# Kernel optimization log

Hardware: AMD Instinct MI355X
Metric: run time of the kernel (lower is better)

The kernel has to match this reference:

```python
import jax, jax.numpy as jnp
import numpy as np

H = 64  # hidden size

def setup_inputs() -> dict:
    key = jax.random.key(0)
    ks = jax.random.split(key, 10)
    B, T = 8192, 256
    s = 1.0 / np.sqrt(H)  # torch LSTM/Linear init scale
    x = jax.random.normal(ks[0], (B, T, 1), dtype=jnp.float32)
    W_ih = jax.random.uniform(ks[1], (4 * H, 1), minval=-s, maxval=s, dtype=jnp.float32)
    W_hh = jax.random.uniform(ks[2], (4 * H, H), minval=-s, maxval=s, dtype=jnp.float32)
    b_ih = jax.random.uniform(ks[3], (4 * H,), minval=-s, maxval=s, dtype=jnp.float32)
    b_hh = jax.random.uniform(ks[4], (4 * H,), minval=-s, maxval=s, dtype=jnp.float32)
    fc1_w = jax.random.uniform(ks[5], (32, H), minval=-s, maxval=s, dtype=jnp.float32)
    fc1_b = jax.random.uniform(ks[6], (32,), minval=-s, maxval=s, dtype=jnp.float32)
    s2 = 1.0 / np.sqrt(32)
    fc2_w = jax.random.uniform(ks[7], (2, 32), minval=-s2, maxval=s2, dtype=jnp.float32)
    fc2_b = jax.random.uniform(ks[8], (2,), minval=-s2, maxval=s2, dtype=jnp.float32)
    return {"x": x, "W_ih": W_ih, "W_hh": W_hh, "b_ih": b_ih, "b_hh": b_hh,
            "fc1_w": fc1_w, "fc1_b": fc1_b, "fc2_w": fc2_w, "fc2_b": fc2_b}

def _lstm_last(x, W_ih, W_hh, b_ih, b_hh):
    # x: [B, T, 1]; returns final hidden state h_T: [B, H]
    B = x.shape[0]
    b = b_ih + b_hh
    x_t = jnp.swapaxes(x, 0, 1)  # [T, B, 1]
    # input contribution precomputed for all steps: [T, B, 4H]
    xg = jnp.einsum('tbi,gi->tbg', x_t, W_ih) + b
    def step(carry, xg_t):
        h, c = carry
        gates = xg_t + h @ W_hh.T  # [B, 4H]
        i, f, g, o = jnp.split(gates, 4, axis=-1)  # torch gate order i,f,g,o
        i = jax.nn.sigmoid(i); f = jax.nn.sigmoid(f)
        g = jnp.tanh(g); o = jax.nn.sigmoid(o)
        c = f * c + i * g
        h = o * jnp.tanh(c)
        return (h, c), None
    h0 = jnp.zeros((B, H), dtype=x.dtype)
    c0 = jnp.zeros((B, H), dtype=x.dtype)
    (h, _), _ = jax.lax.scan(step, (h0, c0), xg)
    return h

def reference(x, W_ih, W_hh, b_ih, b_hh, fc1_w, fc1_b, fc2_w, fc2_b):
    h = _lstm_last(x, W_ih, W_hh, b_ih, b_hh)          # lstm_out[:, -1, :] == h_n
    z = jax.nn.relu(h @ fc1_w.T + fc1_b)               # fc1 + relu
    return z @ fc2_w.T + fc2_b                          # fc2 -> [B, 2]
```

## Files before the change

kernel.cpp:

```cpp
#include <hip/hip_runtime.h>


typedef __attribute__((ext_vector_type(8))) _Float16 f16x8;
typedef __attribute__((ext_vector_type(4))) float f32x4;

#define TT 256
#define BT 16
#define XPAD 260

#if __has_builtin(__builtin_amdgcn_exp2f)
#define EXP2F __builtin_amdgcn_exp2f
#else
#define EXP2F exp2f
#endif
#if __has_builtin(__builtin_amdgcn_rcpf)
#define RCPF __builtin_amdgcn_rcpf
#else
#define RCPF(x) (1.0f / (x))
#endif
#if __has_builtin(__builtin_amdgcn_fmed3f)
#define MED3F __builtin_amdgcn_fmed3f
#else
#define MED3F(a, lo, hi) fminf(fmaxf((a), (lo)), (hi))
#endif

#define NLOG2E  -1.4426950408889634f
#define N2LOG2E -2.8853900817779268f

__device__ __forceinline__ ushort f2h_bits(float f) {
    union { _Float16 h; ushort u; } v;
    v.h = (_Float16)f;
    return v.u;
}
__device__ __forceinline__ float h2f(ushort u) {
    union { ushort u; _Float16 h; } v;
    v.u = u;
    return (float)v.h;
}

__global__ __launch_bounds__(1024, 8) void lstm_h16(
    const float* __restrict__ x,
    const float* __restrict__ W_ih,
    const float* __restrict__ W_hh,
    const float* __restrict__ b_ih,
    const float* __restrict__ b_hh,
    const float* __restrict__ fc1_w,
    const float* __restrict__ fc1_b,
    const float* __restrict__ fc2_w,
    const float* __restrict__ fc2_b,
    float* __restrict__ out)
{
    __shared__ float  x_lds[BT][XPAD];
    __shared__ ushort h_pl[2][BT * 64];

    const int tid  = threadIdx.x;
    const int lane = tid & 63;
    const int w    = tid >> 6;
    const int l15  = lane & 15;
    const int l4   = lane >> 4;
    const int s7   = l15 & 7;
    const long long bBase = (long long)blockIdx.x * BT;

    {
        const float4* xg = (const float4*)(x + bBase * TT);
        const int b = tid >> 6, c4 = tid & 63;
        *(float4*)&x_lds[b][c4 * 4] = xg[tid];
    }
    h_pl[0][tid] = 0;

    const int gate = l15 & 3;
    const int um   = w * 4 + (l15 >> 2);
    const float sgA = (gate == 2) ? N2LOG2E : NLOG2E;
    f16x8 Wf[2];
#pragma unroll
    for (int kt = 0; kt < 2; ++kt) {
        const float* src = W_hh + (gate * 64 + um) * 64 + kt * 32 + l4 * 8;
#pragma unroll
        for (int j = 0; j < 8; ++j)
            Wf[kt][j] = (_Float16)(src[j] * sgA);
    }

    const int u = 4 * w + l4;
    float wih[4], bias[4];
#pragma unroll
    for (int g = 0; g < 4; ++g) {
        const float sg = (g == 2) ? N2LOG2E : NLOG2E;
        const int idx = g * 64 + u;
        wih[g]  = W_ih[idx] * sg;
        bias[g] = (b_ih[idx] + b_hh[idx]) * sg;
    }

    const int ro = l15 * 64;
    const int b0 = l4 ^ s7;
    const int o0 = ro + b0 * 8;
    const int o1 = ro + (b0 ^ 4) * 8;
    const int wo = ro + (((w >> 1) ^ s7) << 3) + ((w & 1) << 2) + l4;

    float cst = 0.0f;
    __syncthreads();

    auto step = [&](int p, int t) {
        const f16x8 bh0 = *(const f16x8*)&h_pl[p][o0];
        const f16x8 bh1 = *(const f16x8*)&h_pl[p][o1];
        const float xr = x_lds[l15][t];

        f32x4 acc;
#pragma unroll
        for (int g = 0; g < 4; ++g) acc[g] = xr * wih[g] + bias[g];

        acc = __builtin_amdgcn_mfma_f32_16x16x32_f16(Wf[0], bh0, acc, 0, 0, 0);
        acc = __builtin_amdgcn_mfma_f32_16x16x32_f16(Wf[1], bh1, acc, 0, 0, 0);

        const float A  = EXP2F(acc[0]);
        const float F  = EXP2F(acc[1]);
        const float Bv = EXP2F(acc[2]);
        const float C  = EXP2F(acc[3]);
        const float pA = 1.0f + A, pF = 1.0f + F, pB = 1.0f + Bv, pC = 1.0f + C;
        const float P   = pA * pB;
        const float den = P * pF;
        const float num = cst * P + (1.0f - Bv) * pF;
        const float cc  = num * RCPF(den);
        cst = cc;
        const float targ = MED3F(N2LOG2E * cc, -60.0f, 60.0f);
        const float D  = EXP2F(targ);
        const float hn = (1.0f - D) * RCPF(pC * (1.0f + D));

        h_pl[p ^ 1][wo] = f2h_bits(hn);
        __syncthreads();
    };

#pragma unroll 1
    for (int t = 0; t < TT; t += 2) {
        step(0, t);
        step(1, t + 1);
    }

    if (tid < BT * 32) {
        const int b = tid >> 5, u2 = tid & 31;
        float a = fc1_b[u2];
        for (int k = 0; k < 64; ++k) {
            const int off = b * 64 + ((((k >> 3) ^ (b & 7))) << 3) + (k & 7);
            a += fc1_w[u2 * 64 + k] * h2f(h_pl[0][off]);
        }
        x_lds[b][u2] = a > 0.0f ? a : 0.0f;
    }
    __syncthreads();
    if (tid < BT * 2) {
        const int b = tid >> 1, o = tid & 1;
        float a = fc2_b[o];
#pragma unroll
        for (int u2 = 0; u2 < 32; ++u2)
            a += x_lds[b][u2] * fc2_w[o * 32 + u2];
        out[(bBase + b) * 2 + o] = a;
    }
}

extern "C" void kernel_launch(void* const* d_in, const int* in_sizes, int n_in,
                              void* d_out, int out_size, void* d_ws, size_t ws_size,
                              hipStream_t stream) {
    const float* x     = (const float*)d_in[0];
    const float* W_ih  = (const float*)d_in[1];
    const float* W_hh  = (const float*)d_in[2];
    const float* b_ih  = (const float*)d_in[3];
    const float* b_hh  = (const float*)d_in[4];
    const float* fc1_w = (const float*)d_in[5];
    const float* fc1_b = (const float*)d_in[6];
    const float* fc2_w = (const float*)d_in[7];
    const float* fc2_b = (const float*)d_in[8];
    float* out = (float*)d_out;

    lstm_h16<<<dim3(8192 / BT), dim3(1024), 0, stream>>>(
        x, W_ih, W_hh, b_ih, b_hh, fc1_w, fc1_b, fc2_w, fc2_b, out);
}
```

Measured before the change: 160.5 us.

## Switch LSTM recurrence to 32x32x16 MFMA with 32-sequence blocks

Each block now handles 32 batch rows with 512 threads (8 waves) and uses the 32x32x16 f16 MFMA. Each wave computes 8 hidden units by 4 gates for all 32 rows, so one lane now processes four cell states per step. This halves the number of blocks and per-step barriers relative to the work done, and amortises the LDS h reads over more rows. In exchange each thread carries more registers and does a longer serial gate computation per step, and each block syncs 8 waves instead of 16 per timestep.

```diff
diff --git a/kernel.cpp b/kernel.cpp
--- a/kernel.cpp
+++ b/kernel.cpp
@@ -2,10 +2,10 @@
 
 
 typedef __attribute__((ext_vector_type(8))) _Float16 f16x8;
-typedef __attribute__((ext_vector_type(4))) float f32x4;
+typedef __attribute__((ext_vector_type(16))) float f32x16;
 
 #define TT 256
-#define BT 16
+#define BT 32
 #define XPAD 260
 
 #if __has_builtin(__builtin_amdgcn_exp2f)
@@ -38,7 +38,7 @@
     return (float)v.h;
 }
 
-__global__ __launch_bounds__(1024, 8) void lstm_h16(
+__global__ __launch_bounds__(512, 2) void lstm_32(
     const float* __restrict__ x,
     const float* __restrict__ W_ih,
     const float* __restrict__ W_hh,
@@ -56,93 +56,110 @@
     const int tid  = threadIdx.x;
     const int lane = tid & 63;
     const int w    = tid >> 6;
-    const int l15  = lane & 15;
-    const int l4   = lane >> 4;
-    const int s7   = l15 & 7;
+    const int b31  = lane & 31;
+    const int hi   = lane >> 5;
+    const int s7   = b31 & 7;
     const long long bBase = (long long)blockIdx.x * BT;
 
     {
         const float4* xg = (const float4*)(x + bBase * TT);
-        const int b = tid >> 6, c4 = tid & 63;
-        *(float4*)&x_lds[b][c4 * 4] = xg[tid];
+        for (int i = tid; i < BT * TT / 4; i += 512) {
+            int b = i >> 6, c4 = i & 63;
+            *(float4*)&x_lds[b][c4 * 4] = xg[i];
+        }
     }
-    h_pl[0][tid] = 0;
+    ((unsigned long long*)h_pl[0])[tid] = 0ull;
 
-    const int gate = l15 & 3;
-    const int um   = w * 4 + (l15 >> 2);
-    const float sgA = (gate == 2) ? N2LOG2E : NLOG2E;
-    f16x8 Wf[2];
+    const int gateA = b31 & 3;
+    const int unitA = 8 * w + (b31 >> 2);
+    const float sgA = (gateA == 2) ? N2LOG2E : NLOG2E;
+    f16x8 Af[4];
 #pragma unroll
-    for (int kt = 0; kt < 2; ++kt) {
-        const float* src = W_hh + (gate * 64 + um) * 64 + kt * 32 + l4 * 8;
+    for (int kt = 0; kt < 4; ++kt) {
+        const float* src = W_hh + (gateA * 64 + unitA) * 64 + kt * 16 + hi * 8;
 #pragma unroll
         for (int j = 0; j < 8; ++j)
-            Wf[kt][j] = (_Float16)(src[j] * sgA);
+            Af[kt][j] = (_Float16)(src[j] * sgA);
     }
 
-    const int u = 4 * w + l4;
-    float wih[4], bias[4];
+    float wih[16], bias[16];
 #pragma unroll
-    for (int g = 0; g < 4; ++g) {
+    for (int r = 0; r < 16; ++r) {
+        const int g = r & 3, q = r >> 2;
+        const int u = 8 * w + 2 * q + hi;
         const float sg = (g == 2) ? N2LOG2E : NLOG2E;
         const int idx = g * 64 + u;
-        wih[g]  = W_ih[idx] * sg;
-        bias[g] = (b_ih[idx] + b_hh[idx]) * sg;
+        wih[r]  = W_ih[idx] * sg;
+        bias[r] = (b_ih[idx] + b_hh[idx]) * sg;
     }
 
-    const int ro = l15 * 64;
-    const int b0 = l4 ^ s7;
-    const int o0 = ro + b0 * 8;
-    const int o1 = ro + (b0 ^ 4) * 8;
-    const int wo = ro + (((w >> 1) ^ s7) << 3) + ((w & 1) << 2) + l4;
+    const int ro = b31 * 64;
+    int rdOff[4], wrOff[4];
+#pragma unroll
+    for (int kt = 0; kt < 4; ++kt)
+        rdOff[kt] = ro + (((2 * kt + hi) ^ s7) << 3);
+#pragma unroll
+    for (int q = 0; q < 4; ++q)
+        wrOff[q] = ro + ((w ^ s7) << 3) + 2 * q + hi;
 
-    float cst = 0.0f;
+    float cst[4] = {0.f, 0.f, 0.f, 0.f};
     __syncthreads();
 
-    auto step = [&](int p, int t) {
-        const f16x8 bh0 = *(const f16x8*)&h_pl[p][o0];
-        const f16x8 bh1 = *(const f16x8*)&h_pl[p][o1];
-        const float xr = x_lds[l15][t];
+    auto stepf = [&](int p, int t) {
+        const f16x8 B0 = *(const f16x8*)&h_pl[p][rdOff[0]];
+        const f16x8 B1 = *(const f16x8*)&h_pl[p][rdOff[1]];
+        const f16x8 B2 = *(const f16x8*)&h_pl[p][rdOff[2]];
+        const f16x8 B3 = *(const f16x8*)&h_pl[p][rdOff[3]];
+        const float xr = x_lds[b31][t];
 
-        f32x4 acc;
+        f32x16 acc;
 #pragma unroll
-        for (int g = 0; g < 4; ++g) acc[g] = xr * wih[g] + bias[g];
+        for (int r = 0; r < 16; ++r) acc[r] = xr * wih[r] + bias[r];
 
-        acc = __builtin_amdgcn_mfma_f32_16x16x32_f16(Wf[0], bh0, acc, 0, 0, 0);
-        acc = __builtin_amdgcn_mfma_f32_16x16x32_f16(Wf[1], bh1, acc, 0, 0, 0);
+        acc = __builtin_amdgcn_mfma_f32_32x32x16_f16(Af[0], B0, acc, 0, 0, 0);
+        acc = __builtin_amdgcn_mfma_f32_32x32x16_f16(Af[1], B1, acc, 0, 0, 0);
+        acc = __builtin_amdgcn_mfma_f32_32x32x16_f16(Af[2], B2, acc, 0, 0, 0);
+        acc = __builtin_amdgcn_mfma_f32_32x32x16_f16(Af[3], B3, acc, 0, 0, 0);
 
-        const float A  = EXP2F(acc[0]);
-        const float F  = EXP2F(acc[1]);
-        const float Bv = EXP2F(acc[2]);
-        const float C  = EXP2F(acc[3]);
-        const float pA = 1.0f + A, pF = 1.0f + F, pB = 1.0f + Bv, pC = 1.0f + C;
-        const float P   = pA * pB;
-        const float den = P * pF;
-        const float num = cst * P + (1.0f - Bv) * pF;
-        const float cc  = num * RCPF(den);
-        cst = cc;
-        const float targ = MED3F(N2LOG2E * cc, -60.0f, 60.0f);
-        const float D  = EXP2F(targ);
-        const float hn = (1.0f - D) * RCPF(pC * (1.0f + D));
-
-        h_pl[p ^ 1][wo] = f2h_bits(hn);
+#pragma unroll
+        for (int q = 0; q < 4; ++q) {
+            const float A_ = EXP2F(acc[4 * q + 0]);
+            const float F_ = EXP2F(acc[4 * q + 1]);
+            const float Bv = EXP2F(acc[4 * q + 2]);
+            const float C_ = EXP2F(acc[4 * q + 3]);
+            const float pA = 1.0f + A_, pF = 1.0f + F_, pB = 1.0f + Bv, pC = 1.0f + C_;
+            const float P   = pA * pB;
+            const float den = P * pF;
+            const float num = cst[q] * P + (1.0f - Bv) * pF;
+            const float cc  = num * RCPF(den);
+            cst[q] = cc;
+            const float targ = MED3F(N2LOG2E * cc, -60.0f, 60.0f);
+            const float D  = EXP2F(targ);
+            const float hn = (1.0f - D) * RCPF(pC * (1.0f + D));
+            h_pl[p ^ 1][wrOff[q]] = f2h_bits(hn);
+        }
         __syncthreads();
     };
 
 #pragma unroll 1
     for (int t = 0; t < TT; t += 2) {
-        step(0, t);
-        step(1, t + 1);
+        stepf(0, t);
+        stepf(1, t + 1);
     }
 
-    if (tid < BT * 32) {
-        const int b = tid >> 5, u2 = tid & 31;
-        float a = fc1_b[u2];
-        for (int k = 0; k < 64; ++k) {
-            const int off = b * 64 + ((((k >> 3) ^ (b & 7))) << 3) + (k & 7);
-            a += fc1_w[u2 * 64 + k] * h2f(h_pl[0][off]);
+    {
+        const int b = tid >> 4;
+        const int u2a = (tid & 15) * 2;
+#pragma unroll
+        for (int q2 = 0; q2 < 2; ++q2) {
+            const int u2 = u2a + q2;
+            float a = fc1_b[u2];
+            for (int k = 0; k < 64; ++k) {
+                const int off = b * 64 + ((((k >> 3) ^ (b & 7))) << 3) + (k & 7);
+                a += fc1_w[u2 * 64 + k] * h2f(h_pl[0][off]);
+            }
+            x_lds[b][u2] = a > 0.0f ? a : 0.0f;
         }
-        x_lds[b][u2] = a > 0.0f ? a : 0.0f;
     }
     __syncthreads();
     if (tid < BT * 2) {
@@ -169,6 +186,6 @@
     const float* fc2_b = (const float*)d_in[8];
     float* out = (float*)d_out;
 
-    lstm_h16<<<dim3(8192 / BT), dim3(1024), 0, stream>>>(
+    lstm_32<<<dim3(8192 / BT), dim3(512), 0, stream>>>(
         x, W_ih, W_hh, b_ih, b_hh, fc1_w, fc1_b, fc2_w, fc2_b, out);
 }
```

Result: slower. 178.8 us (+11.4%).

## Halve batch tile to 8 rows and use 8-wave blocks with two MFMAs per k-slice

Applied to the files above, without the earlier changes.

Changes the block to 512 threads handling 8 batch rows, so each wave computes 8 hidden units by issuing two MFMA tiles per k-slice. Only half of the 16 MFMA columns now carry useful batch rows, and each lane selects the accumulator it owns. The aim is a shorter per-step barrier over fewer waves and twice as many blocks, which may raise CU occupancy across the 256 serial steps. In exchange, half of the MFMA work is wasted and W_hh fragments double per thread, raising register pressure.

```diff
diff --git a/kernel.cpp b/kernel.cpp
--- a/kernel.cpp
+++ b/kernel.cpp
@@ -5,7 +5,7 @@
 typedef __attribute__((ext_vector_type(4))) float f32x4;
 
 #define TT 256
-#define BT 16
+#define BT 8
 #define XPAD 260
 
 #if __has_builtin(__builtin_amdgcn_exp2f)
@@ -38,7 +38,7 @@
     return (float)v.h;
 }
 
-__global__ __launch_bounds__(1024, 8) void lstm_h16(
+__global__ __launch_bounds__(512, 8) void lstm_g4(
     const float* __restrict__ x,
     const float* __restrict__ W_ih,
     const float* __restrict__ W_hh,
@@ -58,7 +58,8 @@
     const int w    = tid >> 6;
     const int l15  = lane & 15;
     const int l4   = lane >> 4;
-    const int s7   = l15 & 7;
+    const int r    = l15 & 7;
+    const bool own0 = (l15 < 8);
     const long long bBase = (long long)blockIdx.x * BT;
 
     {
@@ -68,54 +69,66 @@
     }
     h_pl[0][tid] = 0;
 
-    const int gate = l15 & 3;
-    const int um   = w * 4 + (l15 >> 2);
-    const float sgA = (gate == 2) ? N2LOG2E : NLOG2E;
-    f16x8 Wf[2];
+    const int gateA = l15 & 3;
+    const float sgA = (gateA == 2) ? N2LOG2E : NLOG2E;
+    f16x8 Af[2][2];
 #pragma unroll
-    for (int kt = 0; kt < 2; ++kt) {
-        const float* src = W_hh + (gate * 64 + um) * 64 + kt * 32 + l4 * 8;
+    for (int tt = 0; tt < 2; ++tt) {
+        const int unit = 8 * w + tt * 4 + (l15 >> 2);
 #pragma unroll
-        for (int j = 0; j < 8; ++j)
-            Wf[kt][j] = (_Float16)(src[j] * sgA);
+        for (int kt = 0; kt < 2; ++kt) {
+            const float* src = W_hh + (gateA * 64 + unit) * 64 + kt * 32 + l4 * 8;
+#pragma unroll
+            for (int j = 0; j < 8; ++j)
+                Af[tt][kt][j] = (_Float16)(src[j] * sgA);
+        }
     }
 
-    const int u = 4 * w + l4;
+    const int unit_o = 8 * w + (own0 ? 0 : 4) + l4;
     float wih[4], bias[4];
 #pragma unroll
     for (int g = 0; g < 4; ++g) {
         const float sg = (g == 2) ? N2LOG2E : NLOG2E;
-        const int idx = g * 64 + u;
+        const int idx = g * 64 + unit_o;
         wih[g]  = W_ih[idx] * sg;
         bias[g] = (b_ih[idx] + b_hh[idx]) * sg;
     }
 
-    const int ro = l15 * 64;
-    const int b0 = l4 ^ s7;
-    const int o0 = ro + b0 * 8;
-    const int o1 = ro + (b0 ^ 4) * 8;
-    const int wo = ro + (((w >> 1) ^ s7) << 3) + ((w & 1) << 2) + l4;
+    const int rd0 = r * 64 + ((l4 ^ r) << 3);
+    const int rd1 = r * 64 + (((4 + l4) ^ r) << 3);
+    const int wo  = r * 64 + ((w ^ r) << 3) + (unit_o & 7);
 
     float cst = 0.0f;
     __syncthreads();
 
-    auto step = [&](int p, int t) {
-        const f16x8 bh0 = *(const f16x8*)&h_pl[p][o0];
-        const f16x8 bh1 = *(const f16x8*)&h_pl[p][o1];
-        const float xr = x_lds[l15][t];
+    auto stepf = [&](int p, int t) {
+        const f16x8 B0 = *(const f16x8*)&h_pl[p][rd0];
+        const f16x8 B1 = *(const f16x8*)&h_pl[p][rd1];
+        const float xr = x_lds[r][t];
 
-        f32x4 acc;
+        f32x4 a0, a1;
 #pragma unroll
-        for (int g = 0; g < 4; ++g) acc[g] = xr * wih[g] + bias[g];
+        for (int g = 0; g < 4; ++g) {
+            const float iv = xr * wih[g] + bias[g];
+            a0[g] = own0 ? iv : 0.0f;
+            a1[g] = own0 ? 0.0f : iv;
+        }
 
-        acc = __builtin_amdgcn_mfma_f32_16x16x32_f16(Wf[0], bh0, acc, 0, 0, 0);
-        acc = __builtin_amdgcn_mfma_f32_16x16x32_f16(Wf[1], bh1, acc, 0, 0, 0);
+        a0 = __builtin_amdgcn_mfma_f32_16x16x32_f16(Af[0][0], B0, a0, 0, 0, 0);
+        a1 = __builtin_amdgcn_mfma_f32_16x16x32_f16(Af[1][0], B0, a1, 0, 0, 0);
+        a0 = __builtin_amdgcn_mfma_f32_16x16x32_f16(Af[0][1], B1, a0, 0, 0, 0);
+        a1 = __builtin_amdgcn_mfma_f32_16x16x32_f16(Af[1][1], B1, a1, 0, 0, 0);
 
-        const float A  = EXP2F(acc[0]);
-        const float F  = EXP2F(acc[1]);
-        const float Bv = EXP2F(acc[2]);
-        const float C  = EXP2F(acc[3]);
-        const float pA = 1.0f + A, pF = 1.0f + F, pB = 1.0f + Bv, pC = 1.0f + C;
+        float pi = own0 ? a0[0] : a1[0];
+        float pf = own0 ? a0[1] : a1[1];
+        float pg = own0 ? a0[2] : a1[2];
+        float po = own0 ? a0[3] : a1[3];
+
+        const float A_ = EXP2F(pi);
+        const float F_ = EXP2F(pf);
+        const float Bv = EXP2F(pg);
+        const float C_ = EXP2F(po);
+        const float pA = 1.0f + A_, pF = 1.0f + F_, pB = 1.0f + Bv, pC = 1.0f + C_;
         const float P   = pA * pB;
         const float den = P * pF;
         const float num = cst * P + (1.0f - Bv) * pF;
@@ -131,15 +144,15 @@
 
 #pragma unroll 1
     for (int t = 0; t < TT; t += 2) {
-        step(0, t);
-        step(1, t + 1);
+        stepf(0, t);
+        stepf(1, t + 1);
     }
 
     if (tid < BT * 32) {
         const int b = tid >> 5, u2 = tid & 31;
         float a = fc1_b[u2];
         for (int k = 0; k < 64; ++k) {
-            const int off = b * 64 + ((((k >> 3) ^ (b & 7))) << 3) + (k & 7);
+            const int off = b * 64 + ((((k >> 3) ^ b)) << 3) + (k & 7);
             a += fc1_w[u2 * 64 + k] * h2f(h_pl[0][off]);
         }
         x_lds[b][u2] = a > 0.0f ? a : 0.0f;
@@ -169,6 +182,6 @@
     const float* fc2_b = (const float*)d_in[8];
     float* out = (float*)d_out;
 
-    lstm_h16<<<dim3(8192 / BT), dim3(1024), 0, stream>>>(
+    lstm_g4<<<dim3(8192 / BT), dim3(512), 0, stream>>>(
         x, W_ih, W_hh, b_ih, b_hh, fc1_w, fc1_b, fc2_w, fc2_b, out);
 }
```

Measured after the change: 217.2 us. 1.35x slower.

## Interleave two independent batch groups per block to overlap MFMA with gate math

Applied to the files above, without the earlier changes.

Each block now handles 32 sequences as two 16-row groups with separate h buffers. The MFMA for one group is issued while the previous group's gate nonlinearities finish, so tensor-core latency overlaps the exp/rcp chain across the barrier. Blocks are halved in count and LDS per block grows, which changes occupancy. The intent is to hide the serial per-step dependency latency that dominated the recurrence.

```diff
diff --git a/kernel.cpp b/kernel.cpp
--- a/kernel.cpp
+++ b/kernel.cpp
@@ -5,7 +5,7 @@
 typedef __attribute__((ext_vector_type(4))) float f32x4;
 
 #define TT 256
-#define BT 16
+#define BT 32
 #define XPAD 260
 
 #if __has_builtin(__builtin_amdgcn_exp2f)
@@ -38,7 +38,7 @@
     return (float)v.h;
 }
 
-__global__ __launch_bounds__(1024, 8) void lstm_h16(
+__global__ __launch_bounds__(1024, 4) void lstm_sk(
     const float* __restrict__ x,
     const float* __restrict__ W_ih,
     const float* __restrict__ W_hh,
@@ -51,7 +51,8 @@
     float* __restrict__ out)
 {
     __shared__ float  x_lds[BT][XPAD];
-    __shared__ ushort h_pl[2][BT * 64];
+    __shared__ ushort hA[16 * 64];
+    __shared__ ushort hB[16 * 64];
 
     const int tid  = threadIdx.x;
     const int lane = tid & 63;
@@ -63,21 +64,24 @@
 
     {
         const float4* xg = (const float4*)(x + bBase * TT);
-        const int b = tid >> 6, c4 = tid & 63;
-        *(float4*)&x_lds[b][c4 * 4] = xg[tid];
+        for (int i = tid; i < BT * TT / 4; i += 1024) {
+            int b = i >> 6, c4 = i & 63;
+            *(float4*)&x_lds[b][c4 * 4] = xg[i];
+        }
     }
-    h_pl[0][tid] = 0;
+    hA[tid] = 0;
+    hB[tid] = 0;
 
-    const int gate = l15 & 3;
-    const int um   = w * 4 + (l15 >> 2);
-    const float sgA = (gate == 2) ? N2LOG2E : NLOG2E;
-    f16x8 Wf[2];
+    const int gateA = l15 & 3;
+    const int unitA = 4 * w + (l15 >> 2);
+    const float sgA = (gateA == 2) ? N2LOG2E : NLOG2E;
+    f16x8 Af[2];
 #pragma unroll
     for (int kt = 0; kt < 2; ++kt) {
-        const float* src = W_hh + (gate * 64 + um) * 64 + kt * 32 + l4 * 8;
+        const float* src = W_hh + (gateA * 64 + unitA) * 64 + kt * 32 + l4 * 8;
 #pragma unroll
         for (int j = 0; j < 8; ++j)
-            Wf[kt][j] = (_Float16)(src[j] * sgA);
+            Af[kt][j] = (_Float16)(src[j] * sgA);
     }
 
     const int u = 4 * w + l4;
@@ -90,57 +94,71 @@
         bias[g] = (b_ih[idx] + b_hh[idx]) * sg;
     }
 
-    const int ro = l15 * 64;
-    const int b0 = l4 ^ s7;
-    const int o0 = ro + b0 * 8;
-    const int o1 = ro + (b0 ^ 4) * 8;
-    const int wo = ro + (((w >> 1) ^ s7) << 3) + ((w & 1) << 2) + l4;
+    const int ro  = l15 * 64;
+    const int rd0 = ro + ((l4 ^ s7) << 3);
+    const int rd1 = ro + (((4 + l4) ^ s7) << 3);
+    const int wo  = ro + (((w >> 1) ^ s7) << 3) + 4 * (w & 1) + l4;
 
-    float cst = 0.0f;
+    auto cell = [&](const f32x4& acc, float& c) -> float {
+        const float A_ = EXP2F(acc[0]);
+        const float F_ = EXP2F(acc[1]);
+        const float Bv = EXP2F(acc[2]);
+        const float C_ = EXP2F(acc[3]);
+        const float pA = 1.0f + A_, pF = 1.0f + F_, pB = 1.0f + Bv, pC = 1.0f + C_;
+        const float P   = pA * pB;
+        const float den = P * pF;
+        const float num = c * P + (1.0f - Bv) * pF;
+        const float cc  = num * RCPF(den);
+        c = cc;
+        const float targ = MED3F(N2LOG2E * cc, -60.0f, 60.0f);
+        const float D = EXP2F(targ);
+        return (1.0f - D) * RCPF(pC * (1.0f + D));
+    };
+
+    float cA = 0.0f, cB = 0.0f;
+    f32x4 accA, accB;
     __syncthreads();
 
-    auto step = [&](int p, int t) {
-        const f16x8 bh0 = *(const f16x8*)&h_pl[p][o0];
-        const f16x8 bh1 = *(const f16x8*)&h_pl[p][o1];
-        const float xr = x_lds[l15][t];
+#pragma unroll 1
+    for (int t = 0; t < TT; ++t) {
+        {
+            const f16x8 B0 = *(const f16x8*)&hA[rd0];
+            const f16x8 B1 = *(const f16x8*)&hA[rd1];
+            const float xr = x_lds[l15][t];
+            f32x4 a;
+#pragma unroll
+            for (int g = 0; g < 4; ++g) a[g] = xr * wih[g] + bias[g];
+            a = __builtin_amdgcn_mfma_f32_16x16x32_f16(Af[0], B0, a, 0, 0, 0);
+            a = __builtin_amdgcn_mfma_f32_16x16x32_f16(Af[1], B1, a, 0, 0, 0);
+            if (t) hB[wo] = f2h_bits(cell(accB, cB));
+            accA = a;
+        }
+        __syncthreads();
+        {
+            const f16x8 B0 = *(const f16x8*)&hB[rd0];
+            const f16x8 B1 = *(const f16x8*)&hB[rd1];
+            const float xr = x_lds[16 + l15][t];
+            f32x4 a;
+#pragma unroll
+            for (int g = 0; g < 4; ++g) a[g] = xr * wih[g] + bias[g];
+            a = __builtin_amdgcn_mfma_f32_16x16x32_f16(Af[0], B0, a, 0, 0, 0);
+            a = __builtin_amdgcn_mfma_f32_16x16x32_f16(Af[1], B1, a, 0, 0, 0);
+            hA[wo] = f2h_bits(cell(accA, cA));
+            accB = a;
+        }
+        __syncthreads();
+    }
+    hB[wo] = f2h_bits(cell(accB, cB));
+    __syncthreads();
 
-        f32x4 acc;
-#pragma unroll
-        for (int g = 0; g < 4; ++g) acc[g] = xr * wih[g] + bias[g];
-
-        acc = __builtin_amdgcn_mfma_f32_16x16x32_f16(Wf[0], bh0, acc, 0, 0, 0);
-        acc = __builtin_amdgcn_mfma_f32_16x16x32_f16(Wf[1], bh1, acc, 0, 0, 0);
-
-        const float A  = EXP2F(acc[0]);
-        const float F  = EXP2F(acc[1]);
-        const float Bv = EXP2F(acc[2]);
-        const float C  = EXP2F(acc[3]);
-        const float pA = 1.0f + A, pF = 1.0f + F, pB = 1.0f + Bv, pC = 1.0f + C;
-        const float P   = pA * pB;
-        const float den = P * pF;
-        const float num = cst * P + (1.0f - Bv) * pF;
-        const float cc  = num * RCPF(den);
-        cst = cc;
-        const float targ = MED3F(N2LOG2E * cc, -60.0f, 60.0f);
-        const float D  = EXP2F(targ);
-        const float hn = (1.0f - D) * RCPF(pC * (1.0f + D));
-
-        h_pl[p ^ 1][wo] = f2h_bits(hn);
-        __syncthreads();
-    };
-
-#pragma unroll 1
-    for (int t = 0; t < TT; t += 2) {
-        step(0, t);
-        step(1, t + 1);
-    }
-
-    if (tid < BT * 32) {
+    {
         const int b = tid >> 5, u2 = tid & 31;
+        const ushort* hp = (b < 16) ? hA : hB;
+        const int br = b & 15;
         float a = fc1_b[u2];
         for (int k = 0; k < 64; ++k) {
-            const int off = b * 64 + ((((k >> 3) ^ (b & 7))) << 3) + (k & 7);
-            a += fc1_w[u2 * 64 + k] * h2f(h_pl[0][off]);
+            const int off = br * 64 + ((((k >> 3) ^ (br & 7))) << 3) + (k & 7);
+            a += fc1_w[u2 * 64 + k] * h2f(hp[off]);
         }
         x_lds[b][u2] = a > 0.0f ? a : 0.0f;
     }
@@ -169,6 +187,6 @@
     const float* fc2_b = (const float*)d_in[8];
     float* out = (float*)d_out;
 
-    lstm_h16<<<dim3(8192 / BT), dim3(1024), 0, stream>>>(
+    lstm_sk<<<dim3(8192 / BT), dim3(1024), 0, stream>>>(
         x, W_ih, W_hh, b_ih, b_hh, fc1_w, fc1_b, fc2_w, fc2_b, out);
 }
```

New measurement: 185.1 us. +15.3%, slower.
